# Performance work log

Measured on AMD Instinct MI355X. Metric: run time of the kernel, lower is better.

## Reference

```python
import jax, jax.numpy as jnp
import numpy as np

B, S, E = 2, 4096, 640
H, D, G = 4, 256, 1      # n_heads, head_dim, n_kv_groups
WINDOW = 512
SCALING = 256.0 ** -0.5  # query_pre_attn_scalar ** -0.5
EPS = 1e-6


def rmsnorm(x, scale):
    # Gemma variant: weight = 1 + scale, computed in fp32 over last dim
    xf = x.astype(jnp.float32)
    var = jnp.mean(xf * xf, axis=-1, keepdims=True)
    return (xf * jax.lax.rsqrt(var + EPS) * (1.0 + scale.astype(jnp.float32))).astype(x.dtype)


def apply_rope(x, cos, sin):
    # x: [B, h, S, D]; cos/sin: [S, D]
    half = x.shape[-1] // 2
    x1, x2 = x[..., :half], x[..., half:]
    rotated = jnp.concatenate([-x2, x1], axis=-1)
    return (x * cos[None, None] + rotated * sin[None, None]).astype(x.dtype)


def setup_inputs() -> dict:
    key = jax.random.key(0)
    ks = jax.random.split(key, 6)
    x = jax.random.normal(ks[0], (B, S, E), dtype=jnp.float32)
    # weights (torch Linear weight.T layout: [in, out])
    Wq = jax.random.normal(ks[1], (E, H * D), dtype=jnp.float32) * 0.02
    Wk = jax.random.normal(ks[2], (E, G * D), dtype=jnp.float32) * 0.02
    Wv = jax.random.normal(ks[3], (E, G * D), dtype=jnp.float32) * 0.02
    Wo = jax.random.normal(ks[4], (H * D, E), dtype=jnp.float32) * 0.02
    q_scale = jnp.zeros((D,), dtype=jnp.float32)
    k_scale = jnp.zeros((D,), dtype=jnp.float32)
    # RoPE tables (theta = rope_local_base = 10000 for sliding layers)
    inv_freq = 1.0 / (10000.0 ** (jnp.arange(0, D, 2, dtype=jnp.float32) / D))
    angles = jnp.arange(S, dtype=jnp.float32)[:, None] * inv_freq[None, :]
    angles = jnp.concatenate([angles, angles], axis=1)  # [S, D]
    cos, sin = jnp.cos(angles), jnp.sin(angles)
    # causal + sliding-window mask; True = masked out
    i = jnp.arange(S)[:, None]
    j = jnp.arange(S)[None, :]
    mask = (j > i) | ((i - j) >= WINDOW)
    return {"x": x, "mask": mask, "cos": cos, "sin": sin,
            "Wq": Wq, "Wk": Wk, "Wv": Wv, "Wo": Wo,
            "q_scale": q_scale, "k_scale": k_scale}


def reference(x, mask, cos, sin, Wq, Wk, Wv, Wo, q_scale, k_scale):
    b, s, _ = x.shape
    q = (x @ Wq).reshape(b, s, H, D).transpose(0, 2, 1, 3)  # [B,H,S,D]
    k = (x @ Wk).reshape(b, s, G, D).transpose(0, 2, 1, 3)  # [B,G,S,D]
    v = (x @ Wv).reshape(b, s, G, D).transpose(0, 2, 1, 3)  # [B,G,S,D]
    q = rmsnorm(q, q_scale)
    k = rmsnorm(k, k_scale)
    q = apply_rope(q, cos, sin)
    k = apply_rope(k, cos, sin)
    # GQA: K/V have G=1 heads; broadcasting replaces repeat_interleave
    scores = (q * SCALING) @ jnp.swapaxes(k, -1, -2)  # [B,H,S,S]
    scores = jnp.where(mask[None, None], -jnp.inf, scores)
    attn = jax.nn.softmax(scores, axis=-1)
    out = attn @ v                                     # [B,H,S,D]
    out = out.transpose(0, 2, 1, 3).reshape(b, s, H * D)
    return out @ Wo
```

## Files before the change

kernel.cpp:

```cpp
#include <hip/hip_runtime.h>
#include <hip/hip_bf16.h>
#include <stdint.h>

#define BB 2
#define SS 4096
#define EE 640
#define HH 4
#define DD 256
#define WIN 512

typedef __attribute__((ext_vector_type(8))) short bv8;
typedef __attribute__((ext_vector_type(4))) float fv4;

__device__ __forceinline__ unsigned short f2b(float f) {
  union { float f; unsigned u; } a; a.f = f;
  unsigned r = a.u + 0x7fffu + ((a.u >> 16) & 1u);
  return (unsigned short)(r >> 16);
}
__device__ __forceinline__ float b2f(unsigned short s) {
  union { unsigned u; float f; } a; a.u = ((unsigned)s) << 16;
  return a.f;
}

typedef const __attribute__((address_space(1))) unsigned int* as1u;
typedef __attribute__((address_space(3))) unsigned int* as3u;
__device__ __forceinline__ void gld16(const unsigned short* g, unsigned short* l) {
  __builtin_amdgcn_global_load_lds((as1u)(const void*)g, (as3u)(void*)l, 16, 0, 0);
}

__global__ __launch_bounds__(256) void k_cast_bf16(const float* __restrict__ src,
                                                   unsigned short* __restrict__ dst, int n4) {
  int i = blockIdx.x * 256 + threadIdx.x;
  if (i >= n4) return;
  fv4 v = ((const fv4*)src)[i];
  ushort4 o; o.x = f2b(v.x); o.y = f2b(v.y); o.z = f2b(v.z); o.w = f2b(v.w);
  ((ushort4*)dst)[i] = o;
}

template <typename T>
__global__ __launch_bounds__(256) void k_transpose_bf16(const T* __restrict__ src,
    unsigned short* __restrict__ dst, int sstride, int dstride) {
  __shared__ float tile[32][33];
  int r0 = blockIdx.x * 32, c0 = blockIdx.y * 32;
  int t = threadIdx.x;
  int rr = t >> 3, cc = (t & 7) * 4;
  const T* p = src + (size_t)(r0 + rr) * sstride + c0 + cc;
  float v[4];
  if constexpr (sizeof(T) == 4) {
    fv4 x = *(const fv4*)p;
    v[0] = x.x; v[1] = x.y; v[2] = x.z; v[3] = x.w;
  } else {
    ushort4 x = *(const ushort4*)p;
    v[0] = b2f(x.x); v[1] = b2f(x.y); v[2] = b2f(x.z); v[3] = b2f(x.w);
  }
#pragma unroll
  for (int i = 0; i < 4; ++i) tile[cc + i][rr] = v[i];
  __syncthreads();
  ushort4 o;
  o.x = f2b(tile[rr][cc + 0]); o.y = f2b(tile[rr][cc + 1]);
  o.z = f2b(tile[rr][cc + 2]); o.w = f2b(tile[rr][cc + 3]);
  *(ushort4*)(dst + (size_t)(c0 + rr) * dstride + r0 + cc) = o;
}

template <bool OUT_BF16>
__global__ __launch_bounds__(256) void k_gemm(const unsigned short* __restrict__ A,
    const unsigned short* __restrict__ Bt, void* __restrict__ Cp,
    int M, int N, int K) {
  __shared__ unsigned short la[128 * 32];
  __shared__ unsigned short lb[128 * 32];
  const int m0 = blockIdx.x * 128, n0 = blockIdx.y * 128;
  const int tid = threadIdx.x, lane = tid & 63, wave = tid >> 6;
  const int wm = (wave >> 1) * 64, wn = (wave & 1) * 64;
  const int g = lane >> 4, lr = lane & 15;
  fv4 acc[4][4] = {};
  const int srow = wave * 32 + (lane >> 2);
  const int sch = (lane & 3) * 8;
  const unsigned short* ga0 = A + (size_t)(m0 + srow) * K + sch;
  const unsigned short* gb0 = Bt + (size_t)(n0 + srow) * K + sch;
  unsigned short* lad = la + wave * 1024;
  unsigned short* lbd = lb + wave * 1024;
  for (int k0 = 0; k0 < K; k0 += 32) {
    __syncthreads();
    gld16(ga0 + k0, lad);
    gld16(ga0 + (size_t)16 * K + k0, lad + 512);
    gld16(gb0 + k0, lbd);
    gld16(gb0 + (size_t)16 * K + k0, lbd + 512);
    __syncthreads();
    bv8 af[4], bf[4];
#pragma unroll
    for (int mi = 0; mi < 4; ++mi) af[mi] = *(const bv8*)(la + (wm + mi * 16 + lr) * 32 + g * 8);
#pragma unroll
    for (int ni = 0; ni < 4; ++ni) bf[ni] = *(const bv8*)(lb + (wn + ni * 16 + lr) * 32 + g * 8);
    __builtin_amdgcn_s_setprio(1);
#pragma unroll
    for (int mi = 0; mi < 4; ++mi)
#pragma unroll
      for (int ni = 0; ni < 4; ++ni)
        acc[mi][ni] = __builtin_amdgcn_mfma_f32_16x16x32_bf16(af[mi], bf[ni], acc[mi][ni], 0, 0, 0);
    __builtin_amdgcn_s_setprio(0);
  }
#pragma unroll
  for (int mi = 0; mi < 4; ++mi) {
#pragma unroll
    for (int r = 0; r < 4; ++r) {
      size_t row = (size_t)(m0 + wm + mi * 16 + g * 4 + r);
#pragma unroll
      for (int ni = 0; ni < 4; ++ni) {
        int col = n0 + wn + ni * 16 + lr;
        float val = acc[mi][ni][r];
        if constexpr (OUT_BF16)
          ((unsigned short*)Cp)[row * N + col] = f2b(val);
        else
          ((float*)Cp)[row * N + col] = val;
      }
    }
  }
}

__global__ __launch_bounds__(320) void k_normrope(const unsigned short* __restrict__ qkv,
    const float* __restrict__ cosp, const float* __restrict__ sinp,
    const float* __restrict__ qsc, const float* __restrict__ ksc,
    unsigned short* __restrict__ qo, unsigned short* __restrict__ ko) {
  int m = blockIdx.x;
  int b = m >> 12, s = m & 4095;
  int wave = threadIdx.x >> 6, lane = threadIdx.x & 63;
  bool isq = wave < 4;
  const unsigned short* src = qkv + (size_t)m * 1536 + (isq ? wave * 256 : 1024);
  const float* scp = isq ? qsc : ksc;
  int d0 = lane * 4;
  ushort4 raw = *(const ushort4*)(src + d0);
  float x0 = b2f(raw.x), x1 = b2f(raw.y), x2 = b2f(raw.z), x3 = b2f(raw.w);
  float ss = x0 * x0 + x1 * x1 + x2 * x2 + x3 * x3;
#pragma unroll
  for (int off = 1; off < 64; off <<= 1) ss += __shfl_xor(ss, off, 64);
  float rs = rsqrtf(ss * (1.0f / 256.0f) + 1e-6f);
  fv4 sc = *(const fv4*)(scp + d0);
  float n0 = x0 * rs * (1.0f + sc.x);
  float n1 = x1 * rs * (1.0f + sc.y);
  float n2 = x2 * rs * (1.0f + sc.z);
  float n3 = x3 * rs * (1.0f + sc.w);
  float p0 = __shfl_xor(n0, 32, 64);
  float p1 = __shfl_xor(n1, 32, 64);
  float p2 = __shfl_xor(n2, 32, 64);
  float p3 = __shfl_xor(n3, 32, 64);
  float sgn = (lane < 32) ? -1.0f : 1.0f;
  fv4 c4 = *(const fv4*)(cosp + (size_t)s * 256 + d0);
  fv4 s4 = *(const fv4*)(sinp + (size_t)s * 256 + d0);
  float mult = isq ? 0.0625f : 1.0f;
  float o0 = (n0 * c4.x + sgn * p0 * s4.x) * mult;
  float o1 = (n1 * c4.y + sgn * p1 * s4.y) * mult;
  float o2 = (n2 * c4.z + sgn * p2 * s4.z) * mult;
  float o3 = (n3 * c4.w + sgn * p3 * s4.w) * mult;
  ushort4 o; o.x = f2b(o0); o.y = f2b(o1); o.z = f2b(o2); o.w = f2b(o3);
  unsigned short* dst = isq
      ? qo + ((size_t)(b * HH + wave) * SS + s) * 256 + d0
      : ko + ((size_t)b * SS + s) * 256 + d0;
  *(ushort4*)dst = o;
}

__global__ __launch_bounds__(256, 2) void k_attn(const unsigned short* __restrict__ q,
    const unsigned short* __restrict__ kg, const unsigned short* __restrict__ vtg,
    unsigned short* __restrict__ att) {
  __shared__ unsigned short kt[64 * 264];
  __shared__ unsigned short vl[256 * 72];
  __shared__ unsigned short pl[4][16 * 72];
  const int i0 = blockIdx.x * 64;
  const int h = blockIdx.y, b = blockIdx.z;
  const int tid = threadIdx.x, wave = tid >> 6, lane = tid & 63;
  const int g = lane >> 4, lr = lane & 15;
  const unsigned short* qp = q + ((size_t)(b * HH + h) * SS + i0 + wave * 16 + lr) * 256;
  bv8 qf[8];
#pragma unroll
  for (int kk = 0; kk < 8; ++kk) qf[kk] = *(const bv8*)(qp + kk * 32 + g * 8);
  fv4 po[16] = {};
  float lsp[4] = {0.f, 0.f, 0.f, 0.f};
  const int t0 = (i0 >= WIN) ? ((i0 - WIN + 1) >> 6) : 0;
  const int t1 = i0 >> 6;
  const unsigned short* kb = kg + (size_t)b * SS * 256;
  const unsigned short* vb = vtg + (size_t)b * 256 * SS;
  bv8 ks[8], vs[8];
#define LOADKV(t)                                                              \
  {                                                                            \
    _Pragma("unroll")                                                          \
    for (int r4 = 0; r4 < 8; ++r4) {                                           \
      int c = tid + r4 * 256;                                                  \
      ks[r4] = *(const bv8*)(kb + (size_t)((t) * 64 + (c >> 5)) * 256 + (c & 31) * 8); \
      vs[r4] = *(const bv8*)(vb + (size_t)(c >> 3) * SS + (t) * 64 + (c & 7) * 8);     \
    }                                                                          \
  }
  LOADKV(t0);
  for (int t = t0; t <= t1; ++t) {
    __syncthreads();
#pragma unroll
    for (int r4 = 0; r4 < 8; ++r4) {
      int c = tid + r4 * 256;
      *(bv8*)(kt + (c >> 5) * 264 + (c & 31) * 8) = ks[r4];
      *(bv8*)(vl + (c >> 3) * 72 + (c & 7) * 8) = vs[r4];
    }
    __syncthreads();
    if (t < t1) LOADKV(t + 1);
    fv4 sa[4] = {};
    __builtin_amdgcn_s_setprio(1);
#pragma unroll
    for (int n2 = 0; n2 < 4; ++n2)
#pragma unroll
      for (int kk = 0; kk < 8; ++kk) {
        bv8 kf = *(const bv8*)(kt + (n2 * 16 + lr) * 264 + kk * 32 + g * 8);
        sa[n2] = __builtin_amdgcn_mfma_f32_16x16x32_bf16(qf[kk], kf, sa[n2], 0, 0, 0);
      }
    __builtin_amdgcn_s_setprio(0);
    const int jb = t * 64;
    const bool need_mask = (jb + 63 > i0) || (i0 + 63 - jb >= WIN);
    if (need_mask) {
#pragma unroll
      for (int n2 = 0; n2 < 4; ++n2) {
        int j = jb + n2 * 16 + lr;
#pragma unroll
        for (int r = 0; r < 4; ++r) {
          int row = i0 + wave * 16 + g * 4 + r;
          if (j > row || row - j >= WIN) sa[n2][r] = -1e30f;
        }
      }
    }
#pragma unroll
    for (int n2 = 0; n2 < 4; ++n2)
#pragma unroll
      for (int r = 0; r < 4; ++r) {
        float p = __expf(sa[n2][r] - 16.5f);
        lsp[r] += p;
        pl[wave][(g * 4 + r) * 72 + n2 * 16 + lr] = f2b(p);
      }
    bv8 pf0 = *(const bv8*)(&pl[wave][lr * 72 + g * 8]);
    bv8 pf1 = *(const bv8*)(&pl[wave][lr * 72 + 32 + g * 8]);
    __builtin_amdgcn_s_setprio(1);
#pragma unroll
    for (int n = 0; n < 16; ++n) {
      bv8 vf0 = *(const bv8*)(vl + (n * 16 + lr) * 72 + g * 8);
      po[n] = __builtin_amdgcn_mfma_f32_16x16x32_bf16(pf0, vf0, po[n], 0, 0, 0);
      bv8 vf1 = *(const bv8*)(vl + (n * 16 + lr) * 72 + 32 + g * 8);
      po[n] = __builtin_amdgcn_mfma_f32_16x16x32_bf16(pf1, vf1, po[n], 0, 0, 0);
    }
    __builtin_amdgcn_s_setprio(0);
  }
#pragma unroll
  for (int off = 1; off < 16; off <<= 1)
#pragma unroll
    for (int r = 0; r < 4; ++r) lsp[r] += __shfl_xor(lsp[r], off, 64);
  float inv[4];
#pragma unroll
  for (int r = 0; r < 4; ++r) inv[r] = 1.0f / lsp[r];
#pragma unroll
  for (int r = 0; r < 4; ++r) {
    size_t row = (size_t)i0 + wave * 16 + g * 4 + r;
    unsigned short* op = att + ((size_t)b * SS + row) * 1024 + h * 256 + lr;
#pragma unroll
    for (int n = 0; n < 16; ++n) op[n * 16] = f2b(po[n][r] * inv[r]);
  }
}

extern "C" void kernel_launch(void* const* d_in, const int* in_sizes, int n_in,
                              void* d_out, int out_size, void* d_ws, size_t ws_size,
                              hipStream_t stream) {
  const float* x    = (const float*)d_in[0];
  const float* cosp = (const float*)d_in[2];
  const float* sinp = (const float*)d_in[3];
  const float* Wq   = (const float*)d_in[4];
  const float* Wk   = (const float*)d_in[5];
  const float* Wv   = (const float*)d_in[6];
  const float* Wo   = (const float*)d_in[7];
  const float* qsc  = (const float*)d_in[8];
  const float* ksc  = (const float*)d_in[9];
  float* out = (float*)d_out;
  char* ws = (char*)d_ws;

  unsigned short* xb   = (unsigned short*)(ws);
  unsigned short* wqkv = (unsigned short*)(ws + 10485760);
  unsigned short* wo   = (unsigned short*)(ws + 12451840);
  unsigned short* qkv  = (unsigned short*)(ws + 13762560);
  unsigned short* qb   = (unsigned short*)(ws + 38928384);
  unsigned short* kbuf = (unsigned short*)(ws + 55705600);
  unsigned short* vt   = (unsigned short*)(ws + 59899904);
  unsigned short* attb = (unsigned short*)(ws + 64094208);

  k_cast_bf16<<<5120, 256, 0, stream>>>(x, xb, 1310720);
  k_transpose_bf16<float><<<dim3(20, 32), 256, 0, stream>>>(Wq, wqkv, 1024, 640);
  k_transpose_bf16<float><<<dim3(20, 8), 256, 0, stream>>>(Wk, wqkv + 1024 * 640, 256, 640);
  k_transpose_bf16<float><<<dim3(20, 8), 256, 0, stream>>>(Wv, wqkv + 1280 * 640, 256, 640);
  k_transpose_bf16<float><<<dim3(32, 20), 256, 0, stream>>>(Wo, wo, 640, 1024);
  k_gemm<true><<<dim3(64, 12), 256, 0, stream>>>(xb, wqkv, qkv, 8192, 1536, 640);
  k_normrope<<<8192, 320, 0, stream>>>(qkv, cosp, sinp, qsc, ksc, qb, kbuf);
  k_transpose_bf16<unsigned short><<<dim3(128, 8), 256, 0, stream>>>(qkv + 1280, vt, 1536, 4096);
  k_transpose_bf16<unsigned short><<<dim3(128, 8), 256, 0, stream>>>(
      qkv + (size_t)4096 * 1536 + 1280, vt + (size_t)256 * 4096, 1536, 4096);
  k_attn<<<dim3(64, 4, 2), 256, 0, stream>>>(qb, kbuf, vt, attb);
  k_gemm<false><<<dim3(64, 5), 256, 0, stream>>>(attb, wo, out, 8192, 640, 1024);
}
```

Baseline: 124.3 us.

## Async double-buffer K in attention, read V from global, retile GEMMs with swizzled grid

The attention kernel now stages K tiles into a double-buffered, XOR-swizzled LDS buffer through direct global-to-LDS loads, replacing the register round-trip. V fragments are read straight from global memory instead of LDS, and the occupancy hint is dropped. The 1D grid is ordered so blocks for the same query range across heads and batches run together, sharing K/V in cache. GEMMs get a 1D grid with an XCD-aware block remap, and the output projection uses 128x64 tiles to put more blocks on the GPU. The risks are extra global-memory latency on the V loads and higher register pressure.

```diff
diff --git a/kernel.cpp b/kernel.cpp
--- a/kernel.cpp
+++ b/kernel.cpp
@@ -62,45 +62,50 @@
   *(ushort4*)(dst + (size_t)(c0 + rr) * dstride + r0 + cc) = o;
 }
 
-template <bool OUT_BF16>
+template <bool OUT_BF16, int BN>
 __global__ __launch_bounds__(256) void k_gemm(const unsigned short* __restrict__ A,
     const unsigned short* __restrict__ Bt, void* __restrict__ Cp,
-    int M, int N, int K) {
+    int M, int N, int K, int nt_n) {
   __shared__ unsigned short la[128 * 32];
-  __shared__ unsigned short lb[128 * 32];
-  const int m0 = blockIdx.x * 128, n0 = blockIdx.y * 128;
+  __shared__ unsigned short lb[BN * 32];
+  const int bid = blockIdx.x;
+  const int gidx = (bid & 7) * (gridDim.x >> 3) + (bid >> 3);
+  const int m0 = (gidx / nt_n) * 128, n0 = (gidx % nt_n) * BN;
   const int tid = threadIdx.x, lane = tid & 63, wave = tid >> 6;
-  const int wm = (wave >> 1) * 64, wn = (wave & 1) * 64;
   const int g = lane >> 4, lr = lane & 15;
-  fv4 acc[4][4] = {};
+  constexpr int MI = (BN == 128) ? 4 : 2;
+  const int wm = (BN == 128) ? (wave >> 1) * 64 : wave * 32;
+  const int wn = (BN == 128) ? (wave & 1) * 64 : 0;
+  fv4 acc[MI][4] = {};
   const int srow = wave * 32 + (lane >> 2);
   const int sch = (lane & 3) * 8;
   const unsigned short* ga0 = A + (size_t)(m0 + srow) * K + sch;
-  const unsigned short* gb0 = Bt + (size_t)(n0 + srow) * K + sch;
   unsigned short* lad = la + wave * 1024;
-  unsigned short* lbd = lb + wave * 1024;
+  const int srowb = (BN == 128) ? srow : (wave * 16 + (lane >> 2));
+  const unsigned short* gb0 = Bt + (size_t)(n0 + srowb) * K + sch;
+  unsigned short* lbd = lb + ((BN == 128) ? wave * 1024 : wave * 512);
   for (int k0 = 0; k0 < K; k0 += 32) {
     __syncthreads();
     gld16(ga0 + k0, lad);
     gld16(ga0 + (size_t)16 * K + k0, lad + 512);
     gld16(gb0 + k0, lbd);
-    gld16(gb0 + (size_t)16 * K + k0, lbd + 512);
+    if constexpr (BN == 128) gld16(gb0 + (size_t)16 * K + k0, lbd + 512);
     __syncthreads();
-    bv8 af[4], bf[4];
-#pragma unroll
-    for (int mi = 0; mi < 4; ++mi) af[mi] = *(const bv8*)(la + (wm + mi * 16 + lr) * 32 + g * 8);
+    bv8 af[MI], bf[4];
+#pragma unroll
+    for (int mi = 0; mi < MI; ++mi) af[mi] = *(const bv8*)(la + (wm + mi * 16 + lr) * 32 + g * 8);
 #pragma unroll
     for (int ni = 0; ni < 4; ++ni) bf[ni] = *(const bv8*)(lb + (wn + ni * 16 + lr) * 32 + g * 8);
     __builtin_amdgcn_s_setprio(1);
 #pragma unroll
-    for (int mi = 0; mi < 4; ++mi)
+    for (int mi = 0; mi < MI; ++mi)
 #pragma unroll
       for (int ni = 0; ni < 4; ++ni)
         acc[mi][ni] = __builtin_amdgcn_mfma_f32_16x16x32_bf16(af[mi], bf[ni], acc[mi][ni], 0, 0, 0);
     __builtin_amdgcn_s_setprio(0);
   }
 #pragma unroll
-  for (int mi = 0; mi < 4; ++mi) {
+  for (int mi = 0; mi < MI; ++mi) {
 #pragma unroll
     for (int r = 0; r < 4; ++r) {
       size_t row = (size_t)(m0 + wm + mi * 16 + g * 4 + r);
@@ -158,14 +163,14 @@
   *(ushort4*)dst = o;
 }
 
-__global__ __launch_bounds__(256, 2) void k_attn(const unsigned short* __restrict__ q,
+__global__ __launch_bounds__(256) void k_attn(const unsigned short* __restrict__ q,
     const unsigned short* __restrict__ kg, const unsigned short* __restrict__ vtg,
     unsigned short* __restrict__ att) {
-  __shared__ unsigned short kt[64 * 264];
-  __shared__ unsigned short vl[256 * 72];
+  __shared__ unsigned short kt[2][64 * 256];
   __shared__ unsigned short pl[4][16 * 72];
-  const int i0 = blockIdx.x * 64;
-  const int h = blockIdx.y, b = blockIdx.z;
+  const int plane = blockIdx.x & 7;
+  const int h = plane & 3, b = plane >> 2;
+  const int i0 = (blockIdx.x >> 3) * 64;
   const int tid = threadIdx.x, wave = tid >> 6, lane = tid & 63;
   const int g = lane >> 4, lr = lane & 15;
   const unsigned short* qp = q + ((size_t)(b * HH + h) * SS + i0 + wave * 16 + lr) * 256;
@@ -178,38 +183,34 @@
   const int t1 = i0 >> 6;
   const unsigned short* kb = kg + (size_t)b * SS * 256;
   const unsigned short* vb = vtg + (size_t)b * 256 * SS;
-  bv8 ks[8], vs[8];
-#define LOADKV(t)                                                              \
-  {                                                                            \
-    _Pragma("unroll")                                                          \
-    for (int r4 = 0; r4 < 8; ++r4) {                                           \
-      int c = tid + r4 * 256;                                                  \
-      ks[r4] = *(const bv8*)(kb + (size_t)((t) * 64 + (c >> 5)) * 256 + (c & 31) * 8); \
-      vs[r4] = *(const bv8*)(vb + (size_t)(c >> 3) * SS + (t) * 64 + (c & 7) * 8);     \
-    }                                                                          \
-  }
-  LOADKV(t0);
+#define STAGEK(t, p)                                                          \
+  {                                                                           \
+    const unsigned short* kbase = kb + (size_t)(t) * 64 * 256;                \
+    _Pragma("unroll")                                                         \
+    for (int c = 0; c < 8; ++c) {                                             \
+      int row_ = wave * 16 + c * 2 + (lane >> 5);                             \
+      int sch_ = ((lane & 31) ^ (row_ & 7)) * 8;                              \
+      gld16(kbase + (size_t)row_ * 256 + sch_, &kt[p][(wave * 16 + c * 2) * 256]); \
+    }                                                                         \
+  }
+  STAGEK(t0, 0);
+  int p = 0;
   for (int t = t0; t <= t1; ++t) {
     __syncthreads();
-#pragma unroll
-    for (int r4 = 0; r4 < 8; ++r4) {
-      int c = tid + r4 * 256;
-      *(bv8*)(kt + (c >> 5) * 264 + (c & 31) * 8) = ks[r4];
-      *(bv8*)(vl + (c >> 3) * 72 + (c & 7) * 8) = vs[r4];
-    }
-    __syncthreads();
-    if (t < t1) LOADKV(t + 1);
+    if (t < t1) STAGEK(t + 1, p ^ 1);
+    const int jb = t * 64;
     fv4 sa[4] = {};
     __builtin_amdgcn_s_setprio(1);
 #pragma unroll
-    for (int n2 = 0; n2 < 4; ++n2)
+    for (int n2 = 0; n2 < 4; ++n2) {
+      const int row_ = n2 * 16 + lr;
 #pragma unroll
       for (int kk = 0; kk < 8; ++kk) {
-        bv8 kf = *(const bv8*)(kt + (n2 * 16 + lr) * 264 + kk * 32 + g * 8);
+        bv8 kf = *(const bv8*)(&kt[p][row_ * 256 + (((kk * 4 + g) ^ (row_ & 7)) * 8)]);
         sa[n2] = __builtin_amdgcn_mfma_f32_16x16x32_bf16(qf[kk], kf, sa[n2], 0, 0, 0);
       }
+    }
     __builtin_amdgcn_s_setprio(0);
-    const int jb = t * 64;
     const bool need_mask = (jb + 63 > i0) || (i0 + 63 - jb >= WIN);
     if (need_mask) {
 #pragma unroll
@@ -226,21 +227,23 @@
     for (int n2 = 0; n2 < 4; ++n2)
 #pragma unroll
       for (int r = 0; r < 4; ++r) {
-        float p = __expf(sa[n2][r] - 16.5f);
-        lsp[r] += p;
-        pl[wave][(g * 4 + r) * 72 + n2 * 16 + lr] = f2b(p);
+        float pe = __expf(sa[n2][r] - 16.5f);
+        lsp[r] += pe;
+        pl[wave][(g * 4 + r) * 72 + n2 * 16 + lr] = f2b(pe);
       }
     bv8 pf0 = *(const bv8*)(&pl[wave][lr * 72 + g * 8]);
     bv8 pf1 = *(const bv8*)(&pl[wave][lr * 72 + 32 + g * 8]);
     __builtin_amdgcn_s_setprio(1);
 #pragma unroll
     for (int n = 0; n < 16; ++n) {
-      bv8 vf0 = *(const bv8*)(vl + (n * 16 + lr) * 72 + g * 8);
+      const unsigned short* vp = vb + (size_t)(n * 16 + lr) * SS + jb;
+      bv8 vf0 = *(const bv8*)(vp + g * 8);
       po[n] = __builtin_amdgcn_mfma_f32_16x16x32_bf16(pf0, vf0, po[n], 0, 0, 0);
-      bv8 vf1 = *(const bv8*)(vl + (n * 16 + lr) * 72 + 32 + g * 8);
+      bv8 vf1 = *(const bv8*)(vp + 32 + g * 8);
       po[n] = __builtin_amdgcn_mfma_f32_16x16x32_bf16(pf1, vf1, po[n], 0, 0, 0);
     }
     __builtin_amdgcn_s_setprio(0);
+    p ^= 1;
   }
 #pragma unroll
   for (int off = 1; off < 16; off <<= 1)
@@ -287,11 +290,11 @@
   k_transpose_bf16<float><<<dim3(20, 8), 256, 0, stream>>>(Wk, wqkv + 1024 * 640, 256, 640);
   k_transpose_bf16<float><<<dim3(20, 8), 256, 0, stream>>>(Wv, wqkv + 1280 * 640, 256, 640);
   k_transpose_bf16<float><<<dim3(32, 20), 256, 0, stream>>>(Wo, wo, 640, 1024);
-  k_gemm<true><<<dim3(64, 12), 256, 0, stream>>>(xb, wqkv, qkv, 8192, 1536, 640);
+  k_gemm<true, 128><<<768, 256, 0, stream>>>(xb, wqkv, qkv, 8192, 1536, 640, 12);
   k_normrope<<<8192, 320, 0, stream>>>(qkv, cosp, sinp, qsc, ksc, qb, kbuf);
   k_transpose_bf16<unsigned short><<<dim3(128, 8), 256, 0, stream>>>(qkv + 1280, vt, 1536, 4096);
   k_transpose_bf16<unsigned short><<<dim3(128, 8), 256, 0, stream>>>(
       qkv + (size_t)4096 * 1536 + 1280, vt + (size_t)256 * 4096, 1536, 4096);
-  k_attn<<<dim3(64, 4, 2), 256, 0, stream>>>(qb, kbuf, vt, attb);
-  k_gemm<false><<<dim3(64, 5), 256, 0, stream>>>(attb, wo, out, 8192, 640, 1024);
-}
+  k_attn<<<512, 256, 0, stream>>>(qb, kbuf, vt, attb);
+  k_gemm<false, 64><<<640, 256, 0, stream>>>(attb, wo, out, 8192, 640, 1024, 10);
+}
```

Measured after the change: 177.5 us. 1.43x slower.
